# Optimization experiments

Measured on AMD Instinct MI355X. Metric: run time of the kernel, lower is better.

The kernel has to match this reference:

```python
import jax, jax.numpy as jnp
import numpy as np
import math

B, T, D = 2, 2048, 1024
H, HD = 16, 64
MAX_LEN = 2048


def _build_rope_sin_cos(max_seq, head_dim):
    inv_freq = 1.0 / 10000 ** (jnp.arange(0, head_dim, 2) / head_dim)
    positions = jnp.arange(max_seq)
    sinusoid_inp = jnp.einsum('i,j->ij', positions.astype(jnp.float32), inv_freq.astype(jnp.float32))
    sin = jnp.repeat(jnp.sin(sinusoid_inp), 2, axis=-1)
    cos = jnp.repeat(jnp.cos(sinusoid_inp), 2, axis=-1)
    return sin, cos


def _rotate_half(x):
    x1 = x[..., ::2]
    x2 = x[..., 1::2]
    return jnp.stack((-x2, x1), axis=-1).reshape(x.shape)


def setup_inputs() -> dict:
    key = jax.random.key(0)
    ks = jax.random.split(key, 6)
    x = jax.random.normal(ks[0], (B, T, D), dtype=jnp.float32)
    # causal boolean mask (B, T, T)
    mask = jnp.broadcast_to(jnp.tril(jnp.ones((T, T), dtype=bool)), (B, T, T))
    s = 1.0 / math.sqrt(D)
    wq = jax.random.normal(ks[1], (D, H, HD), dtype=jnp.float32) * s
    wk = jax.random.normal(ks[2], (D, H, HD), dtype=jnp.float32) * s
    wv = jax.random.normal(ks[3], (D, H, HD), dtype=jnp.float32) * s
    wo = jax.random.normal(ks[4], (H * HD, D), dtype=jnp.float32) * (1.0 / math.sqrt(H * HD))
    return {"x": x, "mask": mask, "wq": wq, "wk": wk, "wv": wv, "wo": wo}


def reference(x, mask, wq, wk, wv, wo):
    Bx, Tx, Dx = x.shape
    # q/k/v projections: DenseGeneral D -> (H, HD)
    q = jnp.einsum('btd,dhe->bthe', x, wq)
    k = jnp.einsum('btd,dhe->bthe', x, wk)
    v = jnp.einsum('btd,dhe->bthe', x, wv)
    sin, cos = _build_rope_sin_cos(MAX_LEN, HD)
    sin_t = sin[:Tx][None, :, None, :]
    cos_t = cos[:Tx][None, :, None, :]
    q = q * cos_t + _rotate_half(q) * sin_t
    k = k * cos_t + _rotate_half(k) * sin_t
    q = jnp.transpose(q, (0, 2, 1, 3))  # (B,H,T,HD)
    k = jnp.transpose(k, (0, 2, 1, 3))
    v = jnp.transpose(v, (0, 2, 1, 3))
    scale = 1.0 / math.sqrt(HD)
    logits = jnp.einsum('bhqd,bhkd->bhqk', q, k) * scale
    mask_f = mask[:, None, :, :].astype(jnp.float32)
    logits = logits + (1.0 - mask_f) * -1e10
    w = jax.nn.softmax(logits, axis=-1)
    attn_out = jnp.einsum('bhqk,bhkd->bhqd', w, v)
    attn_out = jnp.transpose(attn_out, (0, 2, 1, 3)).reshape(Bx, Tx, -1)
    return attn_out @ wo
```

## Files before the change

### kernel.cpp

```cpp
#include <hip/hip_runtime.h>
#include <cstdint>
#include <cstddef>

typedef __bf16 bf16x8 __attribute__((ext_vector_type(8)));
typedef __bf16 bf16x2 __attribute__((ext_vector_type(2)));
typedef float f32x4 __attribute__((ext_vector_type(4)));
typedef float f32x16 __attribute__((ext_vector_type(16)));
typedef unsigned int u32x4 __attribute__((ext_vector_type(4)));
#define UNROLL _Pragma("unroll")

__device__ __forceinline__ unsigned short f2bf(float f) {
  unsigned int x = __builtin_bit_cast(unsigned int, f);
  x += 0x7fffu + ((x >> 16) & 1u);
  return (unsigned short)(x >> 16);
}
__device__ __forceinline__ float bf2f(unsigned short u) {
  return __builtin_bit_cast(float, (unsigned int)u << 16);
}
__device__ __forceinline__ unsigned int cvtpk(float a, float b) {
  bf16x2 t; t[0] = (__bf16)a; t[1] = (__bf16)b;
  return __builtin_bit_cast(unsigned int, t);
}
__device__ __forceinline__ void async16(const void* g, void* l) {
  __builtin_amdgcn_global_load_lds((void __attribute__((address_space(1)))*)g,
                                   (void __attribute__((address_space(3)))*)l,
                                   16, 0, 0);
}

__global__ void prep_all(const float* __restrict__ x,
                         const float* __restrict__ wq, const float* __restrict__ wk,
                         const float* __restrict__ wv, const float* __restrict__ wo,
                         unsigned short* __restrict__ xb,
                         unsigned short* __restrict__ wT,
                         float2* __restrict__ ropetab) {
  __shared__ float tile[32][33];
  const int bx = blockIdx.x, tid = threadIdx.x;
  if (bx < 2048) {
    int i = bx * 256 + tid;
    const float4* p = (const float4*)(x + (size_t)i * 8);
    float4 a = p[0], b = p[1];
    ushort4 o0 = {f2bf(a.x), f2bf(a.y), f2bf(a.z), f2bf(a.w)};
    ushort4 o1 = {f2bf(b.x), f2bf(b.y), f2bf(b.z), f2bf(b.w)};
    ushort4* q = (ushort4*)(xb + (size_t)i * 8);
    q[0] = o0; q[1] = o1;
  } else if (bx < 6144) {
    const int idx = bx - 2048;
    const int z = idx >> 10;
    const float* src = z == 0 ? wq : z == 1 ? wk : z == 2 ? wv : wo;
    unsigned short* dst = wT + (size_t)z * 1048576;
    const int kb = (idx & 31) * 32, nb = ((idx >> 5) & 31) * 32;
    const int c = tid & 31, r4 = (tid >> 5) * 4;
UNROLL
    for (int i = 0; i < 4; ++i)
      tile[r4 + i][c] = src[(size_t)(kb + r4 + i) * 1024 + nb + c];
    __syncthreads();
UNROLL
    for (int i = 0; i < 4; ++i)
      dst[(size_t)(nb + r4 + i) * 1024 + kb + c] = f2bf(tile[c][r4 + i]);
  } else {
    int idx = (bx - 6144) * 256 + tid;
    int t = idx >> 5, i = idx & 31;
    float inv = exp2f(-(float)i * (13.287712379549449f / 32.0f));
    float ang = (float)t * inv;
    ropetab[idx] = make_float2(cosf(ang), sinf(ang));
  }
}

__global__ __launch_bounds__(256, 3) void gemmqkv(
    const unsigned short* __restrict__ A, const unsigned short* __restrict__ Bt,
    unsigned short* __restrict__ qout, unsigned short* __restrict__ kout,
    unsigned short* __restrict__ vtout, const float2* __restrict__ rope) {
  __shared__ __align__(16) unsigned short As[128 * 64];
  __shared__ __align__(16) unsigned short Bs[128 * 64];
  const int tid = threadIdx.x;
  const int lane = tid & 63, wid = tid >> 6;
  const int wr = wid >> 1, wc = wid & 1;
  const int g = lane >> 4, r16 = lane & 15;
  const int m0 = blockIdx.y * 128, n0 = blockIdx.x * 128;

  f32x4 acc[4][4];
UNROLL
  for (int i = 0; i < 4; ++i)
UNROLL
    for (int j = 0; j < 4; ++j) acc[i][j] = (f32x4){0.f, 0.f, 0.f, 0.f};

  const int ce = (((tid & 7) ^ ((tid >> 3) & 7)) << 3);
  const unsigned short* gA = A + (size_t)(m0 + (tid >> 3)) * 1024 + ce;
  const unsigned short* gB = Bt + (size_t)(n0 + (tid >> 3)) * 1024 + ce;
  char* lA = (char*)As + tid * 16;
  char* lB = (char*)Bs + tid * 16;

  const int swz = (r16 & 7) << 4;

  for (int u = 0; u < 16; ++u) {
    const int k0 = u * 64;
UNROLL
    for (int s = 0; s < 4; ++s) {
      async16(gA + (size_t)s * 32 * 1024 + k0, lA + s * 4096);
      async16(gB + (size_t)s * 32 * 1024 + k0, lB + s * 4096);
    }
    __syncthreads();
UNROLL
    for (int kk = 0; kk < 2; ++kk) {
      bf16x8 af[4], bfr[4];
UNROLL
      for (int mi = 0; mi < 4; ++mi)
        af[mi] = *(const bf16x8*)((const char*)As +
                  (wr * 64 + mi * 16 + r16) * 128 + ((kk * 64 + g * 16) ^ swz));
UNROLL
      for (int ni = 0; ni < 4; ++ni)
        bfr[ni] = *(const bf16x8*)((const char*)Bs +
                  (wc * 64 + ni * 16 + r16) * 128 + ((kk * 64 + g * 16) ^ swz));
UNROLL
      for (int mi = 0; mi < 4; ++mi)
UNROLL
        for (int ni = 0; ni < 4; ++ni)
          acc[mi][ni] = __builtin_amdgcn_mfma_f32_16x16x32_bf16(af[mi], bfr[ni],
                                                                acc[mi][ni], 0, 0, 0);
    }
    __syncthreads();
  }

  const int which = n0 >> 10;
  const int b = (m0 >= 2048) ? 1 : 0;
  const float QSCL = 0.18033688011112042f;
UNROLL
  for (int mi = 0; mi < 4; ++mi) {
    const int rowb = m0 + wr * 64 + mi * 16 + g * 4;
    const int trow = rowb & 2047;
UNROLL
    for (int ni = 0; ni < 4; ++ni) {
      const int n = n0 + wc * 64 + ni * 16 + r16;
      const int h = (n >> 6) & 15, e = n & 63;
      f32x4 v = acc[mi][ni];
      if (which < 2) {
        const int fi = e >> 1;
        const bool ev = (e & 1) == 0;
UNROLL
        for (int j = 0; j < 4; ++j) {
          float2 cs = rope[(trow + j) * 32 + fi];
          float p = __shfl_xor(v[j], 1);
          v[j] = ev ? (v[j] * cs.x - p * cs.y) : (v[j] * cs.x + p * cs.y);
        }
        if (which == 0) { v[0] *= QSCL; v[1] *= QSCL; v[2] *= QSCL; v[3] *= QSCL; }
      }
      if (which == 2) {
        size_t base = (((size_t)b * 16 + h) * 64 + e) * 2048 + trow;
        ushort4 pkv = {f2bf(v[0]), f2bf(v[1]), f2bf(v[2]), f2bf(v[3])};
        *(ushort4*)(vtout + base) = pkv;
      } else {
        unsigned short* dst = (which == 0) ? qout : kout;
        size_t base = (((size_t)b * 16 + h) * 2048 + trow) * 64 + e;
UNROLL
        for (int j = 0; j < 4; ++j) dst[base + (size_t)j * 64] = f2bf(v[j]);
      }
    }
  }
}

__global__ __launch_bounds__(256, 4) void gemm_o(
    const unsigned short* __restrict__ A, const unsigned short* __restrict__ Bt,
    float* __restrict__ out) {
  __shared__ __align__(16) unsigned short As[2][64 * 64];
  __shared__ __align__(16) unsigned short Bs[2][64 * 64];
  const int tid = threadIdx.x;
  const int lane = tid & 63, wid = tid >> 6;
  const int wm = wid >> 1, wn = wid & 1;
  const int g = lane >> 4, r16 = lane & 15;
  const int m0 = blockIdx.y * 64, n0 = blockIdx.x * 64;

  f32x4 acc[2][2];
UNROLL
  for (int i = 0; i < 2; ++i)
UNROLL
    for (int j = 0; j < 2; ++j) acc[i][j] = (f32x4){0.f, 0.f, 0.f, 0.f};

  const int ce = (((tid & 7) ^ ((tid >> 3) & 7)) << 3);
  const unsigned short* gA = A + (size_t)(m0 + (tid >> 3)) * 1024 + ce;
  const unsigned short* gB = Bt + (size_t)(n0 + (tid >> 3)) * 1024 + ce;
  const int dst0 = tid * 16;
  const int swz = (r16 & 7) << 4;

#define OSTG(bb, koff) { \
    async16(gA + (koff),             (char*)As[bb] + dst0); \
    async16(gA + 32 * 1024 + (koff), (char*)As[bb] + dst0 + 4096); \
    async16(gB + (koff),             (char*)Bs[bb] + dst0); \
    async16(gB + 32 * 1024 + (koff), (char*)Bs[bb] + dst0 + 4096); }

  OSTG(0, 0)
  for (int u = 0; u < 16; ++u) {
    const int bsel = u & 1;
    if (u + 1 < 16) { OSTG(bsel ^ 1, (u + 1) * 64) }
    __builtin_amdgcn_sched_barrier(0);
    if (u + 1 < 16) { asm volatile("s_waitcnt vmcnt(4)" ::: "memory"); }
    else            { asm volatile("s_waitcnt vmcnt(0)" ::: "memory"); }
    __builtin_amdgcn_s_barrier();
    __builtin_amdgcn_sched_barrier(0);
UNROLL
    for (int kk = 0; kk < 2; ++kk) {
      bf16x8 af[2], bfr[2];
UNROLL
      for (int mi = 0; mi < 2; ++mi)
        af[mi] = *(const bf16x8*)((const char*)As[bsel] +
                  (wm * 32 + mi * 16 + r16) * 128 + ((kk * 64 + g * 16) ^ swz));
UNROLL
      for (int ni = 0; ni < 2; ++ni)
        bfr[ni] = *(const bf16x8*)((const char*)Bs[bsel] +
                  (wn * 32 + ni * 16 + r16) * 128 + ((kk * 64 + g * 16) ^ swz));
UNROLL
      for (int mi = 0; mi < 2; ++mi)
UNROLL
        for (int ni = 0; ni < 2; ++ni)
          acc[mi][ni] = __builtin_amdgcn_mfma_f32_16x16x32_bf16(af[mi], bfr[ni],
                                                                acc[mi][ni], 0, 0, 0);
    }
    __builtin_amdgcn_sched_barrier(0);
    __builtin_amdgcn_s_barrier();
  }
#undef OSTG

UNROLL
  for (int mi = 0; mi < 2; ++mi) {
    const int rowb = m0 + wm * 32 + mi * 16 + g * 4;
UNROLL
    for (int ni = 0; ni < 2; ++ni) {
      const int n = n0 + wn * 32 + ni * 16 + r16;
UNROLL
      for (int j = 0; j < 4; ++j)
        out[(size_t)(rowb + j) * 1024 + n] = acc[mi][ni][j];
    }
  }
}

__device__ const signed char c_qt[32]   = {15,15,10,10,15,14,14,14,13, 9, 9, 4,13,13,12,12, 8, 8,12,11,11,11, 7, 7, 3, 6, 6, 5, 5, 2, 1, 0};
__device__ const signed char c_t0[32]   = { 0,11, 0,11,22, 0,10,20, 0, 0,10, 0,10,19, 0, 9, 0, 9,18, 0, 8,16, 0, 8, 0, 0, 7, 0, 6, 0, 0, 0};
__device__ const signed char c_len[32]  = {11,11,11,11,10,10,10,10,10,10,10,10, 9, 9, 9, 9, 9, 9, 8, 8, 8, 8, 8, 8, 8, 7, 7, 6, 6, 6, 4, 2};
__device__ const signed char c_slot[32] = {24,25,10,11,26,21,22,23,18, 8, 9,-1,19,20,15,16, 6, 7,17,12,13,14, 4, 5,-1, 2, 3, 0, 1,-1,-1,-1};

__global__ __launch_bounds__(256, 2) void attn4(
    const unsigned short* __restrict__ qb, const unsigned short* __restrict__ kb,
    const unsigned short* __restrict__ vtb, unsigned short* __restrict__ attnb,
    unsigned short* __restrict__ po, float* __restrict__ ml) {
  __shared__ __align__(16) char smem[4][16384];
  const int tid = threadIdx.x;
  const int lane = tid & 63, w = tid >> 6;
  const int l31 = lane & 31, h = lane >> 5;
  const int bh = blockIdx.x;
  const int item = blockIdx.y;
  const int qt = c_qt[item];
  const int t0 = c_t0[item];
  const int t1 = t0 + c_len[item];
  const int slot = c_slot[item];
  const int q0w = qt * 128 + w * 32;
  const int qg = q0w + l31;
  const size_t kvbase = (size_t)bh * (2048 * 64);

  bf16x8 qf[4];
  const unsigned short* qp = qb + kvbase + (size_t)qg * 64 + h * 8;
UNROLL
  for (int kk = 0; kk < 4; ++kk) qf[kk] = *(const bf16x8*)(qp + kk * 16);

  u32x4 of; of[0] = of[1] = of[2] = of[3] = 0x3F803F80u;
  const bf16x8 onesf = __builtin_bit_cast(bf16x8, of);

  const int lr = lane >> 3;
  const int cb2 = ((lane & 7) ^ lr) << 3;
  const bool isK = (w < 2);
  const int c0 = isK ? w * 4 : (w - 2) * 4;
  const unsigned short* srcp[4];
  int dstoff[4];
  const size_t step = isK ? 4096 : 64;
UNROLL
  for (int s = 0; s < 4; ++s) {
    int r = (c0 + s) * 8 + lr;
    srcp[s] = isK ? (kb + kvbase + (size_t)r * 64 + cb2)
                  : (vtb + kvbase + (size_t)r * 2048 + cb2);
    dstoff[s] = (w * 4 + s) * 1024 + lane * 16;
  }

  f32x16 o0, o1, lacc;
UNROLL
  for (int r = 0; r < 16; ++r) { o0[r] = 0.f; o1[r] = 0.f; lacc[r] = 0.f; }

#define STAGE_T(tv, bufv) { \
    const int tc_ = ((tv) < t1) ? (tv) : (t1 - 1); \
    char* db_ = &smem[(bufv)][0]; \
    async16(srcp[0] + (size_t)tc_ * step, db_ + dstoff[0]); \
    async16(srcp[1] + (size_t)tc_ * step, db_ + dstoff[1]); \
    async16(srcp[2] + (size_t)tc_ * step, db_ + dstoff[2]); \
    async16(srcp[3] + (size_t)tc_ * step, db_ + dstoff[3]); }

  const int np = (t1 - t0 + 1) >> 1;
  STAGE_T(t0, 0) STAGE_T(t0 + 1, 1)
  if (np > 1) { STAGE_T(t0 + 2, 2) STAGE_T(t0 + 3, 3) }

  const int swz = (l31 & 7) << 4;
  for (int p = 0; p < np; ++p) {
    const int tp = t0 + 2 * p;
    __builtin_amdgcn_sched_barrier(0);
    if (p + 1 < np) { asm volatile("s_waitcnt vmcnt(8)" ::: "memory"); }
    else            { asm volatile("s_waitcnt vmcnt(0)" ::: "memory"); }
    __builtin_amdgcn_s_barrier();
    __builtin_amdgcn_sched_barrier(0);
UNROLL
    for (int sub = 0; sub < 2; ++sub) {
      const int t = tp + sub;
      const int kt0 = t << 6;
      if (t < t1 && kt0 <= q0w + 31) {
        const char* cbuf = &smem[(2 * p + sub) & 3][0];
        f32x16 sa, sb;
UNROLL
        for (int r = 0; r < 16; ++r) { sa[r] = 0.f; sb[r] = 0.f; }
        __builtin_amdgcn_s_setprio(1);
UNROLL
        for (int kk = 0; kk < 4; ++kk) {
          bf16x8 kf = *(const bf16x8*)(cbuf + l31 * 128 + ((kk * 32 + h * 16) ^ swz));
          sa = __builtin_amdgcn_mfma_f32_32x32x16_bf16(kf, qf[kk], sa, 0, 0, 0);
        }
UNROLL
        for (int kk = 0; kk < 4; ++kk) {
          bf16x8 kf = *(const bf16x8*)(cbuf + (32 + l31) * 128 + ((kk * 32 + h * 16) ^ swz));
          sb = __builtin_amdgcn_mfma_f32_32x32x16_bf16(kf, qf[kk], sb, 0, 0, 0);
        }
        __builtin_amdgcn_s_setprio(0);
        if (kt0 + 63 > q0w) {
UNROLL
          for (int r = 0; r < 16; ++r) {
            int koff = (r & 3) + 8 * (r >> 2) + 4 * h;
            if (kt0 + koff > qg) sa[r] = -3e38f;
            if (kt0 + 32 + koff > qg) sb[r] = -3e38f;
          }
        }
UNROLL
        for (int r = 0; r < 16; ++r) {
          sa[r] = exp2f(sa[r]);
          sb[r] = exp2f(sb[r]);
        }
        unsigned int lo[8], hi[8];
UNROLL
        for (int b8 = 0; b8 < 4; ++b8) {
          lo[b8]     = cvtpk(sa[4 * b8], sa[4 * b8 + 1]);
          hi[b8]     = cvtpk(sa[4 * b8 + 2], sa[4 * b8 + 3]);
          lo[4 + b8] = cvtpk(sb[4 * b8], sb[4 * b8 + 1]);
          hi[4 + b8] = cvtpk(sb[4 * b8 + 2], sb[4 * b8 + 3]);
        }
        bf16x8 pa[4];
UNROLL
        for (int j = 0; j < 4; ++j) {
          const int bb = (j >> 1) * 4 + (j & 1) * 2;
          unsigned int a0 = lo[bb], b0 = lo[bb + 1];
          unsigned int a1 = hi[bb], b1 = hi[bb + 1];
          asm volatile("v_permlane32_swap_b32 %0, %1" : "+v"(a0), "+v"(b0));
          asm volatile("v_permlane32_swap_b32 %0, %1" : "+v"(a1), "+v"(b1));
          u32x4 f;
          f[0] = a0; f[1] = a1; f[2] = b0; f[3] = b1;
          pa[j] = __builtin_bit_cast(bf16x8, f);
        }
        __builtin_amdgcn_s_setprio(1);
UNROLL
        for (int j = 0; j < 4; ++j) {
          bf16x8 v0 = *(const bf16x8*)(cbuf + 8192 + l31 * 128 + ((j * 32 + h * 16) ^ swz));
          bf16x8 v1 = *(const bf16x8*)(cbuf + 8192 + (32 + l31) * 128 + ((j * 32 + h * 16) ^ swz));
          o0 = __builtin_amdgcn_mfma_f32_32x32x16_bf16(pa[j], v0, o0, 0, 0, 0);
          o1 = __builtin_amdgcn_mfma_f32_32x32x16_bf16(pa[j], v1, o1, 0, 0, 0);
          lacc = __builtin_amdgcn_mfma_f32_32x32x16_bf16(pa[j], onesf, lacc, 0, 0, 0);
        }
        __builtin_amdgcn_s_setprio(0);
      }
    }
    __builtin_amdgcn_sched_barrier(0);
    __builtin_amdgcn_s_barrier();
    if (p + 2 < np) { STAGE_T(tp + 4, (2 * p) & 3) STAGE_T(tp + 5, (2 * p + 1) & 3) }
  }
#undef STAGE_T

  if (slot < 0) {
    const int b = bh >> 4, hh = bh & 15;
UNROLL
    for (int r = 0; r < 16; ++r) {
      const int qg2 = q0w + (r & 3) + 8 * (r >> 2) + 4 * h;
      const size_t base = (((size_t)b * 2048 + qg2) * 16 + hh) * 64 + l31;
      const float iv = 1.0f / lacc[r];
      attnb[base]      = f2bf(o0[r] * iv);
      attnb[base + 32] = f2bf(o1[r] * iv);
    }
  } else {
    const int p = bh * 27 + slot;
    if (l31 == 0) {
UNROLL
      for (int r = 0; r < 16; ++r)
        ml[p * 128 + w * 32 + (r & 3) + 8 * (r >> 2) + 4 * h] = lacc[r];
    }
    unsigned short* pb = po + (size_t)p * 8192;
UNROLL
    for (int r = 0; r < 16; ++r) {
      const int rl = w * 32 + (r & 3) + 8 * (r >> 2) + 4 * h;
      const float iv = 1.0f / lacc[r];
      pb[rl * 64 + l31]      = f2bf(o0[r] * iv);
      pb[rl * 64 + l31 + 32] = f2bf(o1[r] * iv);
    }
  }
}

__global__ void attn_combine(const unsigned short* __restrict__ po,
                             const float* __restrict__ ml,
                             unsigned short* __restrict__ attnb) {
  const int idx = blockIdx.x * 256 + threadIdx.x;
  const int cg = idx & 3;
  const int row = (idx >> 2) & 127;
  const int t2 = idx >> 9;
  const int qi = t2 % 11;
  const int bh = t2 / 11;
  const int qt = qi + 5;
  const int cnt = (qt < 11) ? 2 : 3;
  const int base = (qt < 11) ? (qt - 5) * 2 : 12 + (qt - 11) * 3;
  const int slotg = bh * 27 + base;
  float acc[16];
UNROLL
  for (int i = 0; i < 16; ++i) acc[i] = 0.f;
  float wsum = 0.f;
  for (int i = 0; i < cnt; ++i) {
    const float l = ml[(slotg + i) * 128 + row];
    wsum += l;
    const ushort4* p = (const ushort4*)(po + (size_t)(slotg + i) * 8192 + row * 64 + cg * 16);
UNROLL
    for (int v = 0; v < 4; ++v) {
      ushort4 u = p[v];
      acc[v * 4 + 0] += l * bf2f(u.x);
      acc[v * 4 + 1] += l * bf2f(u.y);
      acc[v * 4 + 2] += l * bf2f(u.z);
      acc[v * 4 + 3] += l * bf2f(u.w);
    }
  }
  const float inv = 1.0f / wsum;
  const int b = bh >> 4, hh = bh & 15;
  const int q = qt * 128 + row;
  ushort4* out = (ushort4*)(attnb + (((size_t)b * 2048 + q) * 16 + hh) * 64 + cg * 16);
UNROLL
  for (int v = 0; v < 4; ++v) {
    ushort4 o;
    o.x = f2bf(acc[v * 4 + 0] * inv);
    o.y = f2bf(acc[v * 4 + 1] * inv);
    o.z = f2bf(acc[v * 4 + 2] * inv);
    o.w = f2bf(acc[v * 4 + 3] * inv);
    out[v] = o;
  }
}

extern "C" void kernel_launch(void* const* d_in, const int* in_sizes, int n_in,
                              void* d_out, int out_size, void* d_ws, size_t ws_size,
                              hipStream_t stream) {
  (void)in_sizes; (void)n_in; (void)out_size; (void)ws_size;
  const float* x = (const float*)d_in[0];
  const float* wq = (const float*)d_in[2];
  const float* wk = (const float*)d_in[3];
  const float* wv = (const float*)d_in[4];
  const float* wo = (const float*)d_in[5];

  unsigned short* xb = (unsigned short*)d_ws;
  unsigned short* wT = xb + 4 * 1024 * 1024;
  float2* rope = (float2*)(wT + 4 * 1024 * 1024);
  unsigned short* qb = (unsigned short*)(rope + 65536);
  unsigned short* kbuf = qb + 4 * 1024 * 1024;
  unsigned short* vtb = kbuf + 4 * 1024 * 1024;
  unsigned short* attnb = vtb + 4 * 1024 * 1024;

  unsigned short* po = xb;
  float* mlb = (float*)rope;

  prep_all<<<dim3(6400), dim3(256), 0, stream>>>(x, wq, wk, wv, wo, xb, wT, rope);
  gemmqkv<<<dim3(24, 32), dim3(256), 0, stream>>>(xb, wT, qb, kbuf, vtb, rope);
  attn4<<<dim3(32, 32), dim3(256), 0, stream>>>(qb, kbuf, vtb, attnb, po, mlb);
  attn_combine<<<dim3(1024), dim3(256), 0, stream>>>(po, mlb, attnb);
  gemm_o<<<dim3(16, 64), dim3(256), 0, stream>>>(attnb, wT + 3 * 1024 * 1024,
                                                 (float*)d_out);
}
```

Measured before the change: 108.0 us.

## Issue both tiles' QK MFMAs before softmax to overlap exp with matrix work

The per-pair loop body is split into QK, softmax-pack and PV helper lambdas. When both tiles of a pair are valid, the QK products for both tiles are issued back to back, followed by softmax and PV for each tile in turn. The aim is to let the exp and pack work of one tile overlap with in-flight MFMAs and to cut stalls on dependent MFMA results. In exchange it holds two score tile sets live at once, which raises register pressure. It also drops the per-tile causal skip for the second tile, so fully masked tiles now get computed and contribute zero.

```diff
diff --git a/kernel.cpp b/kernel.cpp
--- a/kernel.cpp
+++ b/kernel.cpp
@@ -282,6 +282,65 @@
 UNROLL
   for (int r = 0; r < 16; ++r) { o0[r] = 0.f; o1[r] = 0.f; lacc[r] = 0.f; }
 
+  const int swz = (l31 & 7) << 4;
+
+  auto qkcomp = [&](const char* cbuf, f32x16& sa, f32x16& sb) {
+UNROLL
+    for (int r = 0; r < 16; ++r) { sa[r] = 0.f; sb[r] = 0.f; }
+UNROLL
+    for (int kk = 0; kk < 4; ++kk) {
+      bf16x8 kf = *(const bf16x8*)(cbuf + l31 * 128 + ((kk * 32 + h * 16) ^ swz));
+      sa = __builtin_amdgcn_mfma_f32_32x32x16_bf16(kf, qf[kk], sa, 0, 0, 0);
+    }
+UNROLL
+    for (int kk = 0; kk < 4; ++kk) {
+      bf16x8 kf = *(const bf16x8*)(cbuf + (32 + l31) * 128 + ((kk * 32 + h * 16) ^ swz));
+      sb = __builtin_amdgcn_mfma_f32_32x32x16_bf16(kf, qf[kk], sb, 0, 0, 0);
+    }
+  };
+  auto smpack = [&](f32x16& sa, f32x16& sb, int t, bf16x8* pa) {
+    const int kt0 = t << 6;
+    if (kt0 + 63 > q0w) {
+UNROLL
+      for (int r = 0; r < 16; ++r) {
+        int koff = (r & 3) + 8 * (r >> 2) + 4 * h;
+        if (kt0 + koff > qg) sa[r] = -3e38f;
+        if (kt0 + 32 + koff > qg) sb[r] = -3e38f;
+      }
+    }
+UNROLL
+    for (int r = 0; r < 16; ++r) { sa[r] = exp2f(sa[r]); sb[r] = exp2f(sb[r]); }
+    unsigned int lo[8], hi[8];
+UNROLL
+    for (int b8 = 0; b8 < 4; ++b8) {
+      lo[b8]     = cvtpk(sa[4 * b8], sa[4 * b8 + 1]);
+      hi[b8]     = cvtpk(sa[4 * b8 + 2], sa[4 * b8 + 3]);
+      lo[4 + b8] = cvtpk(sb[4 * b8], sb[4 * b8 + 1]);
+      hi[4 + b8] = cvtpk(sb[4 * b8 + 2], sb[4 * b8 + 3]);
+    }
+UNROLL
+    for (int j = 0; j < 4; ++j) {
+      const int bb = (j >> 1) * 4 + (j & 1) * 2;
+      unsigned int a0 = lo[bb], b0 = lo[bb + 1];
+      unsigned int a1 = hi[bb], b1 = hi[bb + 1];
+      asm volatile("v_permlane32_swap_b32 %0, %1" : "+v"(a0), "+v"(b0));
+      asm volatile("v_permlane32_swap_b32 %0, %1" : "+v"(a1), "+v"(b1));
+      u32x4 f;
+      f[0] = a0; f[1] = a1; f[2] = b0; f[3] = b1;
+      pa[j] = __builtin_bit_cast(bf16x8, f);
+    }
+  };
+  auto pvcomp = [&](const char* cbuf, const bf16x8* pa) {
+UNROLL
+    for (int j = 0; j < 4; ++j) {
+      bf16x8 v0 = *(const bf16x8*)(cbuf + 8192 + l31 * 128 + ((j * 32 + h * 16) ^ swz));
+      bf16x8 v1 = *(const bf16x8*)(cbuf + 8192 + (32 + l31) * 128 + ((j * 32 + h * 16) ^ swz));
+      o0 = __builtin_amdgcn_mfma_f32_32x32x16_bf16(pa[j], v0, o0, 0, 0, 0);
+      o1 = __builtin_amdgcn_mfma_f32_32x32x16_bf16(pa[j], v1, o1, 0, 0, 0);
+      lacc = __builtin_amdgcn_mfma_f32_32x32x16_bf16(pa[j], onesf, lacc, 0, 0, 0);
+    }
+  };
+
 #define STAGE_T(tv, bufv) { \
     const int tc_ = ((tv) < t1) ? (tv) : (t1 - 1); \
     char* db_ = &smem[(bufv)][0]; \
@@ -294,7 +353,6 @@
   STAGE_T(t0, 0) STAGE_T(t0 + 1, 1)
   if (np > 1) { STAGE_T(t0 + 2, 2) STAGE_T(t0 + 3, 3) }
 
-  const int swz = (l31 & 7) << 4;
   for (int p = 0; p < np; ++p) {
     const int tp = t0 + 2 * p;
     __builtin_amdgcn_sched_barrier(0);
@@ -302,71 +360,33 @@
     else            { asm volatile("s_waitcnt vmcnt(0)" ::: "memory"); }
     __builtin_amdgcn_s_barrier();
     __builtin_amdgcn_sched_barrier(0);
-UNROLL
-    for (int sub = 0; sub < 2; ++sub) {
-      const int t = tp + sub;
-      const int kt0 = t << 6;
-      if (t < t1 && kt0 <= q0w + 31) {
-        const char* cbuf = &smem[(2 * p + sub) & 3][0];
-        f32x16 sa, sb;
-UNROLL
-        for (int r = 0; r < 16; ++r) { sa[r] = 0.f; sb[r] = 0.f; }
-        __builtin_amdgcn_s_setprio(1);
-UNROLL
-        for (int kk = 0; kk < 4; ++kk) {
-          bf16x8 kf = *(const bf16x8*)(cbuf + l31 * 128 + ((kk * 32 + h * 16) ^ swz));
-          sa = __builtin_amdgcn_mfma_f32_32x32x16_bf16(kf, qf[kk], sa, 0, 0, 0);
-        }
-UNROLL
-        for (int kk = 0; kk < 4; ++kk) {
-          bf16x8 kf = *(const bf16x8*)(cbuf + (32 + l31) * 128 + ((kk * 32 + h * 16) ^ swz));
-          sb = __builtin_amdgcn_mfma_f32_32x32x16_bf16(kf, qf[kk], sb, 0, 0, 0);
-        }
-        __builtin_amdgcn_s_setprio(0);
-        if (kt0 + 63 > q0w) {
-UNROLL
-          for (int r = 0; r < 16; ++r) {
-            int koff = (r & 3) + 8 * (r >> 2) + 4 * h;
-            if (kt0 + koff > qg) sa[r] = -3e38f;
-            if (kt0 + 32 + koff > qg) sb[r] = -3e38f;
-          }
-        }
-UNROLL
-        for (int r = 0; r < 16; ++r) {
-          sa[r] = exp2f(sa[r]);
-          sb[r] = exp2f(sb[r]);
-        }
-        unsigned int lo[8], hi[8];
-UNROLL
-        for (int b8 = 0; b8 < 4; ++b8) {
-          lo[b8]     = cvtpk(sa[4 * b8], sa[4 * b8 + 1]);
-          hi[b8]     = cvtpk(sa[4 * b8 + 2], sa[4 * b8 + 3]);
-          lo[4 + b8] = cvtpk(sb[4 * b8], sb[4 * b8 + 1]);
-          hi[4 + b8] = cvtpk(sb[4 * b8 + 2], sb[4 * b8 + 3]);
-        }
-        bf16x8 pa[4];
-UNROLL
-        for (int j = 0; j < 4; ++j) {
-          const int bb = (j >> 1) * 4 + (j & 1) * 2;
-          unsigned int a0 = lo[bb], b0 = lo[bb + 1];
-          unsigned int a1 = hi[bb], b1 = hi[bb + 1];
-          asm volatile("v_permlane32_swap_b32 %0, %1" : "+v"(a0), "+v"(b0));
-          asm volatile("v_permlane32_swap_b32 %0, %1" : "+v"(a1), "+v"(b1));
-          u32x4 f;
-          f[0] = a0; f[1] = a1; f[2] = b0; f[3] = b1;
-          pa[j] = __builtin_bit_cast(bf16x8, f);
-        }
-        __builtin_amdgcn_s_setprio(1);
-UNROLL
-        for (int j = 0; j < 4; ++j) {
-          bf16x8 v0 = *(const bf16x8*)(cbuf + 8192 + l31 * 128 + ((j * 32 + h * 16) ^ swz));
-          bf16x8 v1 = *(const bf16x8*)(cbuf + 8192 + (32 + l31) * 128 + ((j * 32 + h * 16) ^ swz));
-          o0 = __builtin_amdgcn_mfma_f32_32x32x16_bf16(pa[j], v0, o0, 0, 0, 0);
-          o1 = __builtin_amdgcn_mfma_f32_32x32x16_bf16(pa[j], v1, o1, 0, 0, 0);
-          lacc = __builtin_amdgcn_mfma_f32_32x32x16_bf16(pa[j], onesf, lacc, 0, 0, 0);
-        }
-        __builtin_amdgcn_s_setprio(0);
-      }
+    const char* cb0 = &smem[(2 * p) & 3][0];
+    const char* cb1 = &smem[(2 * p + 1) & 3][0];
+    if (tp + 1 < t1) {
+      f32x16 sa0, sb0, sa1, sb1;
+      bf16x8 pa0[4], pa1[4];
+      __builtin_amdgcn_s_setprio(1);
+      qkcomp(cb0, sa0, sb0);
+      qkcomp(cb1, sa1, sb1);
+      __builtin_amdgcn_s_setprio(0);
+      smpack(sa0, sb0, tp, pa0);
+      __builtin_amdgcn_s_setprio(1);
+      pvcomp(cb0, pa0);
+      __builtin_amdgcn_s_setprio(0);
+      smpack(sa1, sb1, tp + 1, pa1);
+      __builtin_amdgcn_s_setprio(1);
+      pvcomp(cb1, pa1);
+      __builtin_amdgcn_s_setprio(0);
+    } else if ((tp << 6) <= q0w + 31) {
+      f32x16 sa, sb;
+      bf16x8 pa[4];
+      __builtin_amdgcn_s_setprio(1);
+      qkcomp(cb0, sa, sb);
+      __builtin_amdgcn_s_setprio(0);
+      smpack(sa, sb, tp, pa);
+      __builtin_amdgcn_s_setprio(1);
+      pvcomp(cb0, pa);
+      __builtin_amdgcn_s_setprio(0);
     }
     __builtin_amdgcn_sched_barrier(0);
     __builtin_amdgcn_s_barrier();
```

Result: slower. 110.3 us (+2.1%).
